# Kernel optimization log

Measured on AMD Instinct MI355X. Metric: run time of the kernel, lower is better.

The kernel has to match this reference:

```python
import jax, jax.numpy as jnp
import numpy as np

N = 10000
IN_DIM = 512
OUT_DIM = 128
E = 262144


def setup_inputs() -> dict:
    key = jax.random.key(0)
    ks = jax.random.split(key, 7)
    x = jax.random.normal(ks[0], (N, IN_DIM), dtype=jnp.float32)
    adj = jax.random.uniform(ks[1], (N, N), dtype=jnp.float32) * (1.0 / N)
    # xavier-ish scaled params
    weight = jax.random.normal(ks[2], (IN_DIM, OUT_DIM), dtype=jnp.float32) * (1.0 / np.sqrt(IN_DIM))
    weight_two = jax.random.normal(ks[3], (2 * OUT_DIM, OUT_DIM), dtype=jnp.float32) * (1.0 / np.sqrt(2 * OUT_DIM))
    weight_three = jax.random.normal(ks[4], (2 * OUT_DIM, 1), dtype=jnp.float32) * (1.0 / np.sqrt(2 * OUT_DIM))
    train_edges = jax.random.randint(ks[5], (E, 2), 0, N, dtype=jnp.int32)
    train_false_edges = jax.random.randint(ks[6], (E, 2), 0, N, dtype=jnp.int32)
    return {
        "x": x,
        "adj": adj,
        "weight": weight,
        "weight_two": weight_two,
        "weight_three": weight_three,
        "train_edges": train_edges,
        "train_false_edges": train_false_edges,
    }


def reference(x, adj, weight, weight_two, weight_three, train_edges, train_false_edges):
    # encode: z = adj @ (x @ W)   -> [N, OUT_DIM]
    z = adj @ (x @ weight)
    # decode: vectorized per-edge gather of both endpoints
    edges = jnp.concatenate([train_edges, train_false_edges], axis=0)  # [2E, 2]
    zi = z[edges[:, 0]]  # [2E, OUT_DIM]
    zj = z[edges[:, 1]]  # [2E, OUT_DIM]
    z_pair = jnp.concatenate([zi, zj], axis=1)          # [2E, 2*OUT_DIM]
    z_mult = zi * zj                                     # [2E, OUT_DIM]
    z_pair = jax.nn.relu(z_pair) @ weight_two            # [2E, OUT_DIM]
    logits = jnp.concatenate([z_pair, z_mult], axis=1) @ weight_three  # [2E, 1]
    return jax.nn.sigmoid(logits)
```

## Files before the change

### kernel.cpp

```cpp
#include <hip/hip_runtime.h>

#define N_NODES 10000
#define IN_DIM  512
#define OUT_DIM 128
#define NE      262144
#define K_DIM   10000
#define HT_S    10048

#define BM 64
#define BN 128
#define BK 64
#define SPLITS 8
#define KSTEPS_TOTAL 157
#define STEPS_PER_SPLIT 20

typedef __attribute__((ext_vector_type(8))) __bf16 bf16x8;
typedef __attribute__((ext_vector_type(4))) float  f32x4;

__device__ inline ushort f2bf(float f) {
    uint u = __float_as_uint(f);
    return (ushort)((u + 0x7fffu + ((u >> 16) & 1u)) >> 16);
}
__device__ inline float bf2f(ushort s) {
    return __uint_as_float(((uint)s) << 16);
}
__device__ inline float bflo(uint u) { return __uint_as_float(u << 16); }
__device__ inline float bfhi(uint u) { return __uint_as_float(u & 0xffff0000u); }

__device__ __forceinline__ void gl2lds16(const void* g, void* l) {
    __builtin_amdgcn_global_load_lds(
        (const __attribute__((address_space(1))) void*)g,
        (__attribute__((address_space(3))) void*)l, 16, 0, 0);
}

__global__ __launch_bounds__(256) void k_prep(const float* __restrict__ w,
                                              const float* __restrict__ w2,
                                              const float* __restrict__ w3,
                                              ushort* __restrict__ WT,
                                              float* __restrict__ v,
                                              ushort* __restrict__ hT) {
    const int t = threadIdx.x;
    for (int idx = blockIdx.x * 256 + t; idx < IN_DIM * OUT_DIM; idx += gridDim.x * 256) {
        int k = idx >> 7, n = idx & 127;
        WT[n * IN_DIM + k] = f2bf(w[idx]);
    }
    if (blockIdx.x == 0) {
        float s = 0.f;
        for (int j = 0; j < OUT_DIM; ++j) s += w2[t * OUT_DIM + j] * w3[j];
        v[t] = s;
    }
    if (blockIdx.x == 1) {
        for (int idx = t; idx < 128 * (HT_S - N_NODES); idx += 256) {
            int c = idx / (HT_S - N_NODES), r = idx % (HT_S - N_NODES);
            hT[(size_t)c * HT_S + N_NODES + r] = 0;
        }
    }
}

__global__ __launch_bounds__(256) void k_xw(const float* __restrict__ x,
                                            const ushort* __restrict__ WT,
                                            ushort* __restrict__ hT) {
    const int tid = threadIdx.x, wave = tid >> 6, lane = tid & 63;
    const int lr = lane & 15, lg = lane >> 4;
    const int r0 = blockIdx.x * 16;
    const int c0 = wave * 32;
    const float* pA = x + (size_t)(r0 + lr) * IN_DIM;

    f32x4 acc[2];
#pragma unroll
    for (int nf = 0; nf < 2; ++nf) acc[nf] = (f32x4){0.f, 0.f, 0.f, 0.f};

#pragma unroll
    for (int st = 0; st < 8; ++st) {
        const int k0 = st * 64;
        bf16x8 abf[2];
#pragma unroll
        for (int kh = 0; kh < 2; ++kh) {
            float4 a0 = *(const float4*)(pA + k0 + kh * 32 + lg * 8);
            float4 a1 = *(const float4*)(pA + k0 + kh * 32 + lg * 8 + 4);
            ushort* ap = (ushort*)&abf[kh];
            ap[0] = f2bf(a0.x); ap[1] = f2bf(a0.y); ap[2] = f2bf(a0.z); ap[3] = f2bf(a0.w);
            ap[4] = f2bf(a1.x); ap[5] = f2bf(a1.y); ap[6] = f2bf(a1.z); ap[7] = f2bf(a1.w);
        }
#pragma unroll
        for (int kh = 0; kh < 2; ++kh)
#pragma unroll
            for (int nf = 0; nf < 2; ++nf) {
                bf16x8 bfv = *(const bf16x8*)(WT + (size_t)(c0 + nf * 16 + lr) * IN_DIM + k0 + kh * 32 + lg * 8);
                acc[nf] = __builtin_amdgcn_mfma_f32_16x16x32_bf16(abf[kh], bfv, acc[nf], 0, 0, 0);
            }
    }

    const int m0 = r0 + lg * 4;
#pragma unroll
    for (int nf = 0; nf < 2; ++nf) {
        int c = c0 + nf * 16 + lr;
        ushort4 pk;
        pk.x = f2bf(acc[nf][0]); pk.y = f2bf(acc[nf][1]);
        pk.z = f2bf(acc[nf][2]); pk.w = f2bf(acc[nf][3]);
        *(ushort4*)(hT + (size_t)c * HT_S + m0) = pk;
    }
}

__global__ __launch_bounds__(256) void k_adj(const float* __restrict__ adj,
                                             const ushort* __restrict__ hT,
                                             float* __restrict__ zp) {
    __shared__ ushort Bs[BN * BK];

    const int tid = threadIdx.x, wave = tid >> 6, lane = tid & 63;
    const int lr = lane & 15, lg = lane >> 4;
    const int m0 = blockIdx.x * BM;
    const int split = blockIdx.y;
    const int step0 = split * STEPS_PER_SPLIT;
    const int step1 = min(step0 + STEPS_PER_SPLIT, KSTEPS_TOTAL);

    long  bbase[4];
    char* bldst[4];
#pragma unroll
    for (int q = 0; q < 4; ++q) {
        int c = tid + q * 256;
        int row = c >> 3, ch = c & 7;
        bbase[q] = (long)row * HT_S + (long)((ch ^ (row & 7)) * 8);
        bldst[q] = (char*)Bs + c * 16;
    }

    const int arow = min(m0 + wave * 16 + lr, N_NODES - 1);
    const float* pA = adj + (size_t)arow * K_DIM;

    f32x4 acc[8];
#pragma unroll
    for (int nf = 0; nf < 8; ++nf) acc[nf] = (f32x4){0.f, 0.f, 0.f, 0.f};

    const char* Bb = (const char*)Bs;

    for (int st = step0; st < step1; ++st) {
        const int k0 = st * BK;

#pragma unroll
        for (int q = 0; q < 4; ++q)
            gl2lds16(hT + (bbase[q] + k0), bldst[q]);

        float4 fa[2][2];
#pragma unroll
        for (int kh = 0; kh < 2; ++kh) {
            int kk = k0 + kh * 32 + lg * 8;
            int kc = (kk <= K_DIM - 8) ? kk : (K_DIM - 8);
            fa[kh][0] = *(const float4*)(pA + kc);
            fa[kh][1] = *(const float4*)(pA + kc + 4);
        }

        __syncthreads();

        bf16x8 abf[2];
#pragma unroll
        for (int kh = 0; kh < 2; ++kh) {
            ushort* ap = (ushort*)&abf[kh];
            const float* f0 = (const float*)&fa[kh][0];
#pragma unroll
            for (int e = 0; e < 8; ++e) ap[e] = f2bf(f0[e]);
        }

#pragma unroll
        for (int kh = 0; kh < 2; ++kh)
#pragma unroll
            for (int nf = 0; nf < 8; ++nf) {
                int brow = nf * 16 + lr;
                bf16x8 bv = *(const bf16x8*)(Bb + brow * 128 + ((kh * 64 + lg * 16) ^ ((brow & 7) << 4)));
                acc[nf] = __builtin_amdgcn_mfma_f32_16x16x32_bf16(abf[kh], bv, acc[nf], 0, 0, 0);
            }

        __syncthreads();
    }

    float* out = zp + (size_t)split * N_NODES * OUT_DIM;
    const int orow = m0 + wave * 16 + lg * 4;
#pragma unroll
    for (int nf = 0; nf < 8; ++nf)
#pragma unroll
        for (int r = 0; r < 4; ++r) {
            int row = orow + r;
            if (row < N_NODES)
                out[(size_t)row * OUT_DIM + nf * 16 + lr] = acc[nf][r];
        }
}

__global__ __launch_bounds__(256) void k_node(const float* __restrict__ zp,
                                              const float* __restrict__ v,
                                              float* __restrict__ a,
                                              float* __restrict__ b,
                                              ushort* __restrict__ zb) {
    const int wave = threadIdx.x >> 6, lane = threadIdx.x & 63;
    const int i = blockIdx.x * 4 + wave;
    if (i >= N_NODES) return;
    const int k0 = lane, k1 = lane + 64;

    float z0 = 0.f, z1 = 0.f;
#pragma unroll
    for (int s = 0; s < SPLITS; ++s) {
        const float* row = zp + ((size_t)s * N_NODES + i) * OUT_DIM;
        z0 += row[k0];
        z1 += row[k1];
    }
    zb[(size_t)i * OUT_DIM + k0] = f2bf(z0);
    zb[(size_t)i * OUT_DIM + k1] = f2bf(z1);

    float ra = fmaxf(z0, 0.f) * v[k0] + fmaxf(z1, 0.f) * v[k1];
    float rb = fmaxf(z0, 0.f) * v[OUT_DIM + k0] + fmaxf(z1, 0.f) * v[OUT_DIM + k1];
#pragma unroll
    for (int off = 32; off; off >>= 1) {
        ra += __shfl_down(ra, off);
        rb += __shfl_down(rb, off);
    }
    if (lane == 0) { a[i] = ra; b[i] = rb; }
}

__global__ __launch_bounds__(256) void k_edge(const int* __restrict__ e_true,
                                              const int* __restrict__ e_false,
                                              const float* __restrict__ a,
                                              const float* __restrict__ b,
                                              const ushort* __restrict__ zb,
                                              const float* __restrict__ w3,
                                              float* __restrict__ out) {
    const int lane = threadIdx.x & 63;
    const int grp  = lane >> 4;
    const int l16  = lane & 15;
    const int gw   = (blockIdx.x * blockDim.x + threadIdx.x) >> 6;
    const int nw   = (gridDim.x * blockDim.x) >> 6;

    const float4 wv0 = *(const float4*)(w3 + OUT_DIM + l16 * 8);
    const float4 wv1 = *(const float4*)(w3 + OUT_DIM + l16 * 8 + 4);

    for (int e4 = gw; e4 < (2 * NE) / 4; e4 += nw) {
        const int e = e4 * 4 + grp;
        int2 ij = (e < NE) ? ((const int2*)e_true)[e] : ((const int2*)e_false)[e - NE];
        const int i = ij.x, j = ij.y;

        uint4 zi = *(const uint4*)(zb + (size_t)i * OUT_DIM + l16 * 8);
        uint4 zj = *(const uint4*)(zb + (size_t)j * OUT_DIM + l16 * 8);

        float d;
        d  = wv0.x * bflo(zi.x) * bflo(zj.x);
        d += wv0.y * bfhi(zi.x) * bfhi(zj.x);
        d += wv0.z * bflo(zi.y) * bflo(zj.y);
        d += wv0.w * bfhi(zi.y) * bfhi(zj.y);
        d += wv1.x * bflo(zi.z) * bflo(zj.z);
        d += wv1.y * bfhi(zi.z) * bfhi(zj.z);
        d += wv1.z * bflo(zi.w) * bflo(zj.w);
        d += wv1.w * bfhi(zi.w) * bfhi(zj.w);

#pragma unroll
        for (int off = 8; off; off >>= 1) d += __shfl_xor(d, off, 64);
        if (l16 == 0) {
            float logit = a[i] + b[j] + d;
            out[e] = 1.0f / (1.0f + __expf(-logit));
        }
    }
}

extern "C" void kernel_launch(void* const* d_in, const int* in_sizes, int n_in,
                              void* d_out, int out_size, void* d_ws, size_t ws_size,
                              hipStream_t stream) {
    const float* x      = (const float*)d_in[0];
    const float* adj    = (const float*)d_in[1];
    const float* w      = (const float*)d_in[2];
    const float* w2     = (const float*)d_in[3];
    const float* w3     = (const float*)d_in[4];
    const int* e_true   = (const int*)d_in[5];
    const int* e_false  = (const int*)d_in[6];
    float* out          = (float*)d_out;

    char* ws = (char*)d_ws;
    ushort* hT  = (ushort*)(ws);
    float*  zp  = (float*)(ws + 2572288);
    float*  v   = (float*)(ws + 43532288);
    float*  a   = (float*)(ws + 43533312);
    float*  b   = (float*)(ws + 43573312);
    ushort* zb  = (ushort*)(ws + 43613312);
    ushort* WT  = (ushort*)(ws + 46173312);

    k_prep<<<64, 256, 0, stream>>>(w, w2, w3, WT, v, hT);
    k_xw<<<625, 256, 0, stream>>>(x, WT, hT);
    k_adj<<<dim3(157, SPLITS), 256, 0, stream>>>(adj, hT, zp);
    k_node<<<2500, 256, 0, stream>>>(zp, v, a, b, zb);
    k_edge<<<2048, 256, 0, stream>>>(e_true, e_false, a, b, zb, w3, out);
}
```

Before: 188.7 us.

## Fuse all stages into one persistent cooperative kernel with grid syncs

Folds the five kernels (prep, x@W, adj GEMM, node reduction, edge decode) into a single cooperative-launched persistent kernel that separates phases with grid-wide syncs and loops blocks over tiles. The aim is to remove the four inter-kernel launch gaps and drains. In exchange the grid is capped at 1024 blocks, so the adj GEMM's 1256 tiles no longer fit in one wave. Grid barriers and the loss of per-kernel tuning of grid shape and register use may also cost time. Falls back to the original multi-kernel path if the cooperative launch fails.

```diff
diff --git a/kernel.cpp b/kernel.cpp
--- a/kernel.cpp
+++ b/kernel.cpp
@@ -1,4 +1,7 @@
 #include <hip/hip_runtime.h>
+#include <hip/hip_cooperative_groups.h>
+
+namespace cg = cooperative_groups;
 
 #define N_NODES 10000
 #define IN_DIM  512
@@ -13,6 +16,7 @@
 #define SPLITS 8
 #define KSTEPS_TOTAL 157
 #define STEPS_PER_SPLIT 20
+#define NTILES (157 * SPLITS)
 
 typedef __attribute__((ext_vector_type(8))) __bf16 bf16x8;
 typedef __attribute__((ext_vector_type(4))) float  f32x4;
@@ -20,9 +24,6 @@
 __device__ inline ushort f2bf(float f) {
     uint u = __float_as_uint(f);
     return (ushort)((u + 0x7fffu + ((u >> 16) & 1u)) >> 16);
-}
-__device__ inline float bf2f(ushort s) {
-    return __uint_as_float(((uint)s) << 16);
 }
 __device__ inline float bflo(uint u) { return __uint_as_float(u << 16); }
 __device__ inline float bfhi(uint u) { return __uint_as_float(u & 0xffff0000u); }
@@ -33,36 +34,35 @@
         (__attribute__((address_space(3))) void*)l, 16, 0, 0);
 }
 
-__global__ __launch_bounds__(256) void k_prep(const float* __restrict__ w,
-                                              const float* __restrict__ w2,
-                                              const float* __restrict__ w3,
-                                              ushort* __restrict__ WT,
-                                              float* __restrict__ v,
-                                              ushort* __restrict__ hT) {
-    const int t = threadIdx.x;
-    for (int idx = blockIdx.x * 256 + t; idx < IN_DIM * OUT_DIM; idx += gridDim.x * 256) {
+__device__ __forceinline__ void prep_body(int bid, int nb, int tid,
+                                          const float* __restrict__ w,
+                                          const float* __restrict__ w2,
+                                          const float* __restrict__ w3,
+                                          ushort* __restrict__ WT,
+                                          float* __restrict__ v,
+                                          ushort* __restrict__ hT) {
+    for (int idx = bid * 256 + tid; idx < IN_DIM * OUT_DIM; idx += nb * 256) {
         int k = idx >> 7, n = idx & 127;
         WT[n * IN_DIM + k] = f2bf(w[idx]);
     }
-    if (blockIdx.x == 0) {
+    if (bid == 0) {
         float s = 0.f;
-        for (int j = 0; j < OUT_DIM; ++j) s += w2[t * OUT_DIM + j] * w3[j];
-        v[t] = s;
-    }
-    if (blockIdx.x == 1) {
-        for (int idx = t; idx < 128 * (HT_S - N_NODES); idx += 256) {
+        for (int j = 0; j < OUT_DIM; ++j) s += w2[tid * OUT_DIM + j] * w3[j];
+        v[tid] = s;
+    }
+    if (bid == 1) {
+        for (int idx = tid; idx < 128 * (HT_S - N_NODES); idx += 256) {
             int c = idx / (HT_S - N_NODES), r = idx % (HT_S - N_NODES);
             hT[(size_t)c * HT_S + N_NODES + r] = 0;
         }
     }
 }
 
-__global__ __launch_bounds__(256) void k_xw(const float* __restrict__ x,
-                                            const ushort* __restrict__ WT,
-                                            ushort* __restrict__ hT) {
-    const int tid = threadIdx.x, wave = tid >> 6, lane = tid & 63;
-    const int lr = lane & 15, lg = lane >> 4;
-    const int r0 = blockIdx.x * 16;
+__device__ __forceinline__ void xw_tile(int vb, int wave, int lr, int lg,
+                                        const float* __restrict__ x,
+                                        const ushort* __restrict__ WT,
+                                        ushort* __restrict__ hT) {
+    const int r0 = vb * 16;
     const int c0 = wave * 32;
     const float* pA = x + (size_t)(r0 + lr) * IN_DIM;
 
@@ -102,28 +102,17 @@
     }
 }
 
-__global__ __launch_bounds__(256) void k_adj(const float* __restrict__ adj,
-                                             const ushort* __restrict__ hT,
-                                             float* __restrict__ zp) {
-    __shared__ ushort Bs[BN * BK];
-
-    const int tid = threadIdx.x, wave = tid >> 6, lane = tid & 63;
-    const int lr = lane & 15, lg = lane >> 4;
-    const int m0 = blockIdx.x * BM;
-    const int split = blockIdx.y;
+__device__ __forceinline__ void adj_tile(int t, int tid, int wave, int lr, int lg,
+                                         const long* bbase, char* const* bldst,
+                                         const char* Bb,
+                                         const float* __restrict__ adj,
+                                         const ushort* __restrict__ hT,
+                                         float* __restrict__ zp) {
+    const int mi = t % 157, split = t / 157;
+    const int m0 = mi * BM;
     const int step0 = split * STEPS_PER_SPLIT;
     const int step1 = min(step0 + STEPS_PER_SPLIT, KSTEPS_TOTAL);
 
-    long  bbase[4];
-    char* bldst[4];
-#pragma unroll
-    for (int q = 0; q < 4; ++q) {
-        int c = tid + q * 256;
-        int row = c >> 3, ch = c & 7;
-        bbase[q] = (long)row * HT_S + (long)((ch ^ (row & 7)) * 8);
-        bldst[q] = (char*)Bs + c * 16;
-    }
-
     const int arow = min(m0 + wave * 16 + lr, N_NODES - 1);
     const float* pA = adj + (size_t)arow * K_DIM;
 
@@ -131,11 +120,8 @@
 #pragma unroll
     for (int nf = 0; nf < 8; ++nf) acc[nf] = (f32x4){0.f, 0.f, 0.f, 0.f};
 
-    const char* Bb = (const char*)Bs;
-
     for (int st = step0; st < step1; ++st) {
         const int k0 = st * BK;
-
 #pragma unroll
         for (int q = 0; q < 4; ++q)
             gl2lds16(hT + (bbase[q] + k0), bldst[q]);
@@ -172,7 +158,7 @@
         __syncthreads();
     }
 
-    float* out = zp + (size_t)split * N_NODES * OUT_DIM;
+    float* outp = zp + (size_t)split * N_NODES * OUT_DIM;
     const int orow = m0 + wave * 16 + lg * 4;
 #pragma unroll
     for (int nf = 0; nf < 8; ++nf)
@@ -180,20 +166,17 @@
         for (int r = 0; r < 4; ++r) {
             int row = orow + r;
             if (row < N_NODES)
-                out[(size_t)row * OUT_DIM + nf * 16 + lr] = acc[nf][r];
-        }
-}
-
-__global__ __launch_bounds__(256) void k_node(const float* __restrict__ zp,
-                                              const float* __restrict__ v,
-                                              float* __restrict__ a,
-                                              float* __restrict__ b,
-                                              ushort* __restrict__ zb) {
-    const int wave = threadIdx.x >> 6, lane = threadIdx.x & 63;
-    const int i = blockIdx.x * 4 + wave;
-    if (i >= N_NODES) return;
+                outp[(size_t)row * OUT_DIM + nf * 16 + lr] = acc[nf][r];
+        }
+}
+
+__device__ __forceinline__ void node_body(int i, int lane,
+                                          const float* __restrict__ zp,
+                                          const float* __restrict__ v,
+                                          float* __restrict__ a,
+                                          float* __restrict__ b,
+                                          ushort* __restrict__ zb) {
     const int k0 = lane, k1 = lane + 64;
-
     float z0 = 0.f, z1 = 0.f;
 #pragma unroll
     for (int s = 0; s < SPLITS; ++s) {
@@ -214,19 +197,16 @@
     if (lane == 0) { a[i] = ra; b[i] = rb; }
 }
 
-__global__ __launch_bounds__(256) void k_edge(const int* __restrict__ e_true,
-                                              const int* __restrict__ e_false,
-                                              const float* __restrict__ a,
-                                              const float* __restrict__ b,
-                                              const ushort* __restrict__ zb,
-                                              const float* __restrict__ w3,
-                                              float* __restrict__ out) {
-    const int lane = threadIdx.x & 63;
-    const int grp  = lane >> 4;
-    const int l16  = lane & 15;
-    const int gw   = (blockIdx.x * blockDim.x + threadIdx.x) >> 6;
-    const int nw   = (gridDim.x * blockDim.x) >> 6;
-
+__device__ __forceinline__ void edge_body(int gw, int nw, int lane,
+                                          const int* __restrict__ e_true,
+                                          const int* __restrict__ e_false,
+                                          const float* __restrict__ a,
+                                          const float* __restrict__ b,
+                                          const ushort* __restrict__ zb,
+                                          const float* __restrict__ w3,
+                                          float* __restrict__ out) {
+    const int grp = lane >> 4;
+    const int l16 = lane & 15;
     const float4 wv0 = *(const float4*)(w3 + OUT_DIM + l16 * 8);
     const float4 wv1 = *(const float4*)(w3 + OUT_DIM + l16 * 8 + 4);
 
@@ -255,6 +235,112 @@
             out[e] = 1.0f / (1.0f + __expf(-logit));
         }
     }
+}
+
+__global__ __launch_bounds__(256, 2) void k_mega(
+    const float* __restrict__ x,      const float* __restrict__ adj,
+    const float* __restrict__ w,      const float* __restrict__ w2,
+    const float* __restrict__ w3,     const int* __restrict__ e_true,
+    const int* __restrict__ e_false,  float* __restrict__ out,
+    ushort* __restrict__ hT,          float* __restrict__ zp,
+    float* __restrict__ v,            float* __restrict__ a,
+    float* __restrict__ b,            ushort* __restrict__ zb,
+    ushort* __restrict__ WT)
+{
+    cg::grid_group grid = cg::this_grid();
+    __shared__ ushort Bs[BN * BK];
+
+    const int tid  = threadIdx.x, wave = tid >> 6, lane = tid & 63;
+    const int lr   = lane & 15,   lg   = lane >> 4;
+    const int bid  = blockIdx.x;
+    const int nb   = gridDim.x;
+
+    prep_body(bid, nb, tid, w, w2, w3, WT, v, hT);
+    grid.sync();
+
+    for (int vb = bid; vb < 625; vb += nb)
+        xw_tile(vb, wave, lr, lg, x, WT, hT);
+    grid.sync();
+
+    {
+        long  bbase[4];
+        char* bldst[4];
+#pragma unroll
+        for (int q = 0; q < 4; ++q) {
+            int c = tid + q * 256;
+            int row = c >> 3, ch = c & 7;
+            bbase[q] = (long)row * HT_S + (long)((ch ^ (row & 7)) * 8);
+            bldst[q] = (char*)Bs + c * 16;
+        }
+        for (int t = bid; t < NTILES; t += nb)
+            adj_tile(t, tid, wave, lr, lg, bbase, bldst, (const char*)Bs, adj, hT, zp);
+    }
+    grid.sync();
+
+    for (int nbk = bid; nbk < 2500; nbk += nb)
+        node_body(nbk * 4 + wave, lane, zp, v, a, b, zb);
+    grid.sync();
+
+    edge_body((bid * 256 + tid) >> 6, (nb * 256) >> 6, lane,
+              e_true, e_false, a, b, zb, w3, out);
+}
+
+__global__ __launch_bounds__(256) void k_prep(const float* __restrict__ w,
+                                              const float* __restrict__ w2,
+                                              const float* __restrict__ w3,
+                                              ushort* __restrict__ WT,
+                                              float* __restrict__ v,
+                                              ushort* __restrict__ hT) {
+    prep_body(blockIdx.x, gridDim.x, threadIdx.x, w, w2, w3, WT, v, hT);
+}
+
+__global__ __launch_bounds__(256) void k_xw(const float* __restrict__ x,
+                                            const ushort* __restrict__ WT,
+                                            ushort* __restrict__ hT) {
+    const int tid = threadIdx.x, wave = tid >> 6, lane = tid & 63;
+    xw_tile(blockIdx.x, wave, lane & 15, lane >> 4, x, WT, hT);
+}
+
+__global__ __launch_bounds__(256) void k_adj(const float* __restrict__ adj,
+                                             const ushort* __restrict__ hT,
+                                             float* __restrict__ zp) {
+    __shared__ ushort Bs[BN * BK];
+    const int tid = threadIdx.x, wave = tid >> 6, lane = tid & 63;
+    long  bbase[4];
+    char* bldst[4];
+#pragma unroll
+    for (int q = 0; q < 4; ++q) {
+        int c = tid + q * 256;
+        int row = c >> 3, ch = c & 7;
+        bbase[q] = (long)row * HT_S + (long)((ch ^ (row & 7)) * 8);
+        bldst[q] = (char*)Bs + c * 16;
+    }
+    adj_tile(blockIdx.y * 157 + blockIdx.x, tid, wave, lane & 15, lane >> 4,
+             bbase, bldst, (const char*)Bs, adj, hT, zp);
+}
+
+__global__ __launch_bounds__(256) void k_node(const float* __restrict__ zp,
+                                              const float* __restrict__ v,
+                                              float* __restrict__ a,
+                                              float* __restrict__ b,
+                                              ushort* __restrict__ zb) {
+    const int wave = threadIdx.x >> 6, lane = threadIdx.x & 63;
+    const int i = blockIdx.x * 4 + wave;
+    if (i >= N_NODES) return;
+    node_body(i, lane, zp, v, a, b, zb);
+}
+
+__global__ __launch_bounds__(256) void k_edge(const int* __restrict__ e_true,
+                                              const int* __restrict__ e_false,
+                                              const float* __restrict__ a,
+                                              const float* __restrict__ b,
+                                              const ushort* __restrict__ zb,
+                                              const float* __restrict__ w3,
+                                              float* __restrict__ out) {
+    const int lane = threadIdx.x & 63;
+    const int gw   = (blockIdx.x * blockDim.x + threadIdx.x) >> 6;
+    const int nw   = (gridDim.x * blockDim.x) >> 6;
+    edge_body(gw, nw, lane, e_true, e_false, a, b, zb, w3, out);
 }
 
 extern "C" void kernel_launch(void* const* d_in, const int* in_sizes, int n_in,
@@ -278,9 +364,30 @@
     ushort* zb  = (ushort*)(ws + 43613312);
     ushort* WT  = (ushort*)(ws + 46173312);
 
-    k_prep<<<64, 256, 0, stream>>>(w, w2, w3, WT, v, hT);
-    k_xw<<<625, 256, 0, stream>>>(x, WT, hT);
-    k_adj<<<dim3(157, SPLITS), 256, 0, stream>>>(adj, hT, zp);
-    k_node<<<2500, 256, 0, stream>>>(zp, v, a, b, zb);
-    k_edge<<<2048, 256, 0, stream>>>(e_true, e_false, a, b, zb, w3, out);
-}
+    bool done = false;
+    int occ = 0;
+    hipError_t qerr = hipOccupancyMaxActiveBlocksPerMultiprocessor(
+        &occ, (const void*)k_mega, 256, 0);
+    if (qerr == hipSuccess && occ > 0) {
+        int blocks = occ * 256;
+        if (blocks > 1024) blocks = 1024;
+        const float* xx = x; const float* aj = adj; const float* ww = w;
+        const float* w22 = w2; const float* w33 = w3;
+        const int* et = e_true; const int* ef = e_false; float* oo = out;
+        ushort* hT_ = hT; float* zp_ = zp; float* v_ = v;
+        float* a_ = a; float* b_ = b; ushort* zb_ = zb; ushort* WT_ = WT;
+        void* args[] = { &xx, &aj, &ww, &w22, &w33, &et, &ef, &oo,
+                         &hT_, &zp_, &v_, &a_, &b_, &zb_, &WT_ };
+        hipError_t lerr = hipLaunchCooperativeKernel(
+            (const void*)k_mega, dim3(blocks), dim3(256), args, 0, stream);
+        done = (lerr == hipSuccess);
+    }
+
+    if (!done) {
+        k_prep<<<64, 256, 0, stream>>>(w, w2, w3, WT, v, hT);
+        k_xw<<<625, 256, 0, stream>>>(x, WT, hT);
+        k_adj<<<dim3(157, SPLITS), 256, 0, stream>>>(adj, hT, zp);
+        k_node<<<2500, 256, 0, stream>>>(zp, v, a, b, zb);
+        k_edge<<<2048, 256, 0, stream>>>(e_true, e_false, a, b, zb, w3, out);
+    }
+}
```

Result: slower. 445.1 us (+135.8%).
